# Kernel tuning notes

Hardware: AMD Instinct MI355X
Metric: run time of the kernel (lower is better)

The kernel has to match this reference:

```python
import jax, jax.numpy as jnp
import numpy as np

ITERATIONS = 10      # skil_loss default
BORDER_SIZE = 25     # skil_loss default -> 51-tap gaussian
SIGMA = 10.0         # skil_loss default
LOSS_WEIGHT = 1.0
EPS = 1e-6


def _max_pool3(x):
    # 3x3 max pool, stride 1, SAME padding over last two dims of (N, H, W)
    return jax.lax.reduce_window(x, -jnp.inf, jax.lax.max,
                                 (1, 3, 3), (1, 1, 1), 'SAME')


def _soft_erode(x):
    return -_max_pool3(-x)


def _soft_dilate(x):
    return _max_pool3(x)


def _soft_open(x):
    return _soft_dilate(_soft_erode(x))


def soft_skeletonize(img, iterations):
    # clDice-style iterative soft skeletonization
    skel = jax.nn.relu(img - _soft_open(img))

    def body(carry, _):
        img, skel = carry
        img = _soft_erode(img)
        delta = jax.nn.relu(img - _soft_open(img))
        skel = skel + jax.nn.relu(delta - skel * delta)
        return (img, skel), None

    (img, skel), _ = jax.lax.scan(body, (img, skel), None, length=iterations)
    return skel


def apply_smooth_gaussian_diffusion(x, border_size, sigma):
    # Separable gaussian conv, kernel size 2*border_size+1, peak value 1
    # (soft dilation of the skeleton into a border band), clipped to [0, 1].
    r = jnp.arange(-border_size, border_size + 1, dtype=x.dtype)
    g = jnp.exp(-(r * r) / (2.0 * sigma * sigma))  # peak = 1 at center
    x4 = x[:, None, :, :]  # (N, 1, H, W)
    kh = g.reshape(1, 1, -1, 1)
    kw = g.reshape(1, 1, 1, -1)
    dn = ('NCHW', 'OIHW', 'NCHW')
    y = jax.lax.conv_general_dilated(x4, kh, (1, 1), 'SAME', dimension_numbers=dn)
    y = jax.lax.conv_general_dilated(y, kw, (1, 1), 'SAME', dimension_numbers=dn)
    return jnp.clip(y[:, 0], 0.0, 1.0)


def soft_dice(gt, pr, epsilon=EPS):
    num = 2.0 * jnp.sum(gt * pr, axis=(-2, -1))
    den = jnp.sum(gt * gt, axis=(-2, -1)) + jnp.sum(pr * pr, axis=(-2, -1))
    return (num + epsilon) / (den + epsilon)


def skil_loss(pred_fg, target):
    gt_skel = soft_skeletonize(target, ITERATIONS)
    pr_skel = soft_skeletonize(pred_fg, ITERATIONS)
    gt_border = apply_smooth_gaussian_diffusion(gt_skel, BORDER_SIZE, SIGMA)
    pr_border = apply_smooth_gaussian_diffusion(pr_skel, BORDER_SIZE, SIGMA)
    return 1.0 - soft_dice(gt_border, pr_border)  # (N,)


def setup_inputs() -> dict:
    key = jax.random.key(0)
    k1, k2 = jax.random.split(key)
    pred = jax.random.normal(k1, (8, 2, 1024, 1024), dtype=jnp.float32)
    target = jax.random.uniform(k2, (8, 1024, 1024), dtype=jnp.float32)
    return {"pred": pred, "target": target}


def reference(pred, target):
    # SkilLoss.forward: softmax over classes, foreground channel to skil_loss,
    # weighted_loss 'mean' reduction over batch.
    probs = jax.nn.softmax(pred, axis=1)
    fg = probs[:, 1]  # (N, H, W)
    loss = skil_loss(fg, target)
    return LOSS_WEIGHT * jnp.mean(loss)
```

## Files before the change

### kernel.cpp

```cpp
#include <hip/hip_runtime.h>

#define H 1024
#define W 1024
#define HW (H*W)
#define NB 8
#define NIMG 16
#define BORDER 25
#define KLEN 51

__device__ __constant__ float GW[KLEN] = {
  0.04393693f, 0.05613476f, 0.07100535f, 0.08892162f, 0.11025053f,
  0.13533528f, 0.16447446f, 0.19789869f, 0.23574608f, 0.27803730f,
  0.32465247f, 0.37531110f, 0.42955736f, 0.48675226f, 0.54607442f,
  0.60653066f, 0.66697681f, 0.72614904f, 0.78270454f, 0.83527021f,
  0.88249690f, 0.92311635f, 0.95599748f, 0.98019867f, 0.99501248f,
  1.00000000f,
  0.99501248f, 0.98019867f, 0.95599748f, 0.92311635f, 0.88249690f,
  0.83527021f, 0.78270454f, 0.72614904f, 0.66697681f, 0.60653066f,
  0.54607442f, 0.48675226f, 0.42955736f, 0.37531110f, 0.32465247f,
  0.27803730f, 0.23574608f, 0.19789869f, 0.16447446f, 0.13533528f,
  0.11025053f, 0.08892162f, 0.07100535f, 0.05613476f, 0.04393693f
};

__device__ inline float m3n(float a,float b,float c){
  float d; asm("v_min3_f32 %0, %1, %2, %3" : "=v"(d) : "v"(a), "v"(b), "v"(c));
  return d;
}
__device__ inline float m3x(float a,float b,float c){
  float d; asm("v_max3_f32 %0, %1, %2, %3" : "=v"(d) : "v"(a), "v"(b), "v"(c));
  return d;
}

__device__ inline float dpp_shr1(float x){
  return __int_as_float(__builtin_amdgcn_mov_dpp(__float_as_int(x), 0x138, 0xf, 0xf, true));
}
__device__ inline float dpp_shl1(float x){
  return __int_as_float(__builtin_amdgcn_mov_dpp(__float_as_int(x), 0x130, 0xf, 0xf, true));
}

__device__ inline float4 hmin4(float4 C){
  float Lw = dpp_shr1(C.w);
  float Rx = dpp_shl1(C.x);
  float4 h;
  h.x=m3n(Lw ,C.x,C.y); h.y=m3n(C.x,C.y,C.z);
  h.z=m3n(C.y,C.z,C.w); h.w=m3n(C.z,C.w,Rx );
  return h;
}
__device__ inline float4 hmax4(float4 C){
  float Lw = dpp_shr1(C.w);
  float Rx = dpp_shl1(C.x);
  float4 h;
  h.x=m3x(Lw ,C.x,C.y); h.y=m3x(C.x,C.y,C.z);
  h.z=m3x(C.y,C.z,C.w); h.w=m3x(C.z,C.w,Rx );
  return h;
}
__device__ inline float4 vmin3(float4 a,float4 b,float4 c){
  float4 o; o.x=m3n(a.x,b.x,c.x); o.y=m3n(a.y,b.y,c.y);
            o.z=m3n(a.z,b.z,c.z); o.w=m3n(a.w,b.w,c.w); return o;
}
__device__ inline float4 vmax3(float4 a,float4 b,float4 c){
  float4 o; o.x=m3x(a.x,b.x,c.x); o.y=m3x(a.y,b.y,c.y);
            o.z=m3x(a.z,b.z,c.z); o.w=m3x(a.w,b.w,c.w); return o;
}
__device__ inline float4 msk4(float4 e, bool v){
  constexpr float NINF = -__builtin_huge_valf();
  float4 o; o.x=v?e.x:NINF; o.y=v?e.y:NINF; o.z=v?e.z:NINF; o.w=v?e.w:NINF;
  return o;
}

__global__ __launch_bounds__(512, 4)
void skel11_kernel(const float* __restrict__ pred, const float* __restrict__ targ,
                   float* __restrict__ S, double* __restrict__ sums)
{
  constexpr float PINF = __builtin_huge_valf();
  __shared__ float4 Xch[2][32][32];

  const int img = blockIdx.z;
  const int bx = blockIdx.x, by = blockIdx.y;

  if (bx==0 && by==0 && img==0 && threadIdx.x < 3*NB) sums[threadIdx.x] = 0.0;

  const int gx0 = bx*104 - 12, gy0 = by*72 - 12;
  const int tid = threadIdx.x;
  const int g = tid >> 5;
  const int j = tid & 31;
  const int wid = tid >> 6;
  const int R0 = 6*g;
  const int gxb = gx0 + 4*j;
  const bool xok = ((unsigned)gxb < (unsigned)W);
  const bool cenj = (j >= 3) && (j < 29);
  const bool allok = (gx0 >= 0) && (gx0 + 128 <= W) && (gy0 >= 0) && (gy0 + 96 <= H);
  const bool cwave = (wid >= 1) && (wid <= 6);

  const int ixm = (g>0)  ? 2*g-1 : 0;
  const int ixp = (g<15) ? 2*g+2 : 31;

  float4 I[6], s[6];
  bool yok[6];

  #pragma unroll
  for (int k=0;k<6;++k) {
    int gy = gy0 + R0 + k;
    yok[k] = ((unsigned)gy < (unsigned)H);
    float4 v = make_float4(PINF,PINF,PINF,PINF);
    if (yok[k] && xok) {
      size_t off = (size_t)gy*(W/4) + (gxb>>2);
      if (img < NB) {
        v = ((const float4*)targ)[(size_t)img*(HW/4)+off];
      } else {
        int b2 = img - NB;
        float4 p0 = ((const float4*)pred)[(size_t)(2*b2  )*(HW/4)+off];
        float4 p1 = ((const float4*)pred)[(size_t)(2*b2+1)*(HW/4)+off];
        v.x = 1.0f/(1.0f + expf(p0.x - p1.x));
        v.y = 1.0f/(1.0f + expf(p0.y - p1.y));
        v.z = 1.0f/(1.0f + expf(p0.z - p1.z));
        v.w = 1.0f/(1.0f + expf(p0.w - p1.w));
      }
    }
    I[k] = v;
  }

  #pragma unroll
  for (int u=0; u<11; ++u) {
    float4 h[6];
    #pragma unroll
    for (int k=0;k<6;++k) h[k] = hmin4(I[k]);
    Xch[0][2*g  ][j] = h[0];
    Xch[0][2*g+1][j] = h[5];
    __syncthreads();
    float4 hm = Xch[0][ixm][j];
    float4 hp = Xch[0][ixp][j];
    float4 e[6];
    e[0]=vmin3(hm  ,h[0],h[1]);
    e[1]=vmin3(h[0],h[1],h[2]);
    e[2]=vmin3(h[1],h[2],h[3]);
    e[3]=vmin3(h[2],h[3],h[4]);
    e[4]=vmin3(h[3],h[4],h[5]);
    e[5]=vmin3(h[4],h[5],hp  );

    float4 x[6];
    if (cwave) {
      if (allok) {
        #pragma unroll
        for (int k=0;k<6;++k) x[k] = hmax4(e[k]);
      } else {
        #pragma unroll
        for (int k=0;k<6;++k) x[k] = hmax4(msk4(e[k], xok && yok[k]));
      }
      Xch[1][2*g  ][j] = x[0];
      Xch[1][2*g+1][j] = x[5];
    } else if (wid == 0) {
      float4 x5 = allok ? hmax4(e[5]) : hmax4(msk4(e[5], xok && yok[5]));
      Xch[1][2*g+1][j] = x5;
    } else {
      float4 x0 = allok ? hmax4(e[0]) : hmax4(msk4(e[0], xok && yok[0]));
      Xch[1][2*g  ][j] = x0;
    }
    __syncthreads();

    if (cwave) {
      float4 xm = Xch[1][2*g-1][j];
      float4 xp = Xch[1][2*g+2][j];
      #pragma unroll
      for (int k=0;k<6;++k) {
        float4 dl = vmax3((k==0)?xm:x[k-1], x[k], (k==5)?xp:x[k+1]);
        float dx = fmaxf(I[k].x-dl.x,0.f), dy = fmaxf(I[k].y-dl.y,0.f);
        float dz = fmaxf(I[k].z-dl.z,0.f), dw = fmaxf(I[k].w-dl.w,0.f);
        if (u == 0) {
          s[k] = make_float4(dx,dy,dz,dw);
        } else {
          s[k].x += fmaxf(fmaf(-s[k].x, dx, dx), 0.f);
          s[k].y += fmaxf(fmaf(-s[k].y, dy, dy), 0.f);
          s[k].z += fmaxf(fmaf(-s[k].z, dz, dz), 0.f);
          s[k].w += fmaxf(fmaf(-s[k].w, dw, dw), 0.f);
        }
      }
    }
    #pragma unroll
    for (int k=0;k<6;++k) I[k] = e[k];
  }

  if (cwave && cenj && gxb < W) {
    #pragma unroll
    for (int k=0;k<6;++k) {
      int gy = gy0 + R0 + k;
      if (gy < H)
        ((float4*)S)[(size_t)img*(HW/4) + (size_t)gy*(W/4) + (gxb>>2)] = s[k];
    }
  }
}

__global__ __launch_bounds__(256)
void blur_h_kernel(const float* __restrict__ Sin, float* __restrict__ D)
{
  const int img = blockIdx.y;
  const int y = blockIdx.x;
  const int q = threadIdx.x;
  const float4* src = (const float4*)(Sin + (size_t)img*HW + (size_t)y*W);
  float a0=0.f, a1=0.f, a2=0.f, a3=0.f;
#define ACCUM(val, idx)                                                     \
  { if ((idx)   >= 0 && (idx)   <= 50) a0 += (val) * GW[(idx)];             \
    if ((idx)-1 >= 0 && (idx)-1 <= 50) a1 += (val) * GW[(idx)-1];           \
    if ((idx)-2 >= 0 && (idx)-2 <= 50) a2 += (val) * GW[(idx)-2];           \
    if ((idx)-3 >= 0 && (idx)-3 <= 50) a3 += (val) * GW[(idx)-3]; }
  #pragma unroll
  for (int c = -7; c <= 7; ++c) {
    int qq = q + c;
    float4 v = make_float4(0.f,0.f,0.f,0.f);
    if ((unsigned)qq < 256u) v = src[qq];
    const int base = 4*c + 25;
    ACCUM(v.x, base+0) ACCUM(v.y, base+1) ACCUM(v.z, base+2) ACCUM(v.w, base+3)
  }
#undef ACCUM
  float4 outv; outv.x=a0; outv.y=a1; outv.z=a2; outv.w=a3;
  ((float4*)(D + (size_t)img*HW + (size_t)y*W))[q] = outv;
}

__global__ __launch_bounds__(256)
void blur_v_dice_kernel(const float* __restrict__ D, double* __restrict__ sums)
{
  __shared__ double rbuf[12];
  const int b = blockIdx.z;
  const int gy0 = blockIdx.y * 64;
  const int gx0 = blockIdx.x * 64;
  const int tid = threadIdx.x;
  const int c  = tid & 63;
  const int r0 = gy0 + (tid >> 6) * 16;
  const int x  = gx0 + c;
  const float* gsrc = D + (size_t)b*HW + x;
  const float* psrc = D + (size_t)(b+NB)*HW + x;

  float ag[16], ap[16];
  #pragma unroll
  for (int j = 0; j < 16; ++j) { ag[j] = 0.f; ap[j] = 0.f; }
  #pragma unroll
  for (int t = 0; t < 16 + KLEN - 1; ++t) {
    int gy = r0 - BORDER + t;
    float vg = 0.f, vp = 0.f;
    if ((unsigned)gy < (unsigned)H) {
      size_t a = (size_t)gy*W;
      vg = gsrc[a]; vp = psrc[a];
    }
    #pragma unroll
    for (int j = 0; j < 16; ++j) {
      int k = t - j;
      if (k >= 0 && k < KLEN) { ag[j] += vg * GW[k]; ap[j] += vp * GW[k]; }
    }
  }
  double sgp = 0.0, sgg = 0.0, spp = 0.0;
  #pragma unroll
  for (int j = 0; j < 16; ++j) {
    float a = fminf(fmaxf(ag[j], 0.f), 1.f);
    float p = fminf(fmaxf(ap[j], 0.f), 1.f);
    sgp += (double)(a*p); sgg += (double)(a*a); spp += (double)(p*p);
  }
  #pragma unroll
  for (int off = 32; off > 0; off >>= 1) {
    sgp += __shfl_down(sgp, off);
    sgg += __shfl_down(sgg, off);
    spp += __shfl_down(spp, off);
  }
  int lane = tid & 63, wv = tid >> 6;
  if (lane == 0) { rbuf[wv] = sgp; rbuf[4+wv] = sgg; rbuf[8+wv] = spp; }
  __syncthreads();
  if (tid == 0) {
    double a  = rbuf[0]+rbuf[1]+rbuf[2]+rbuf[3];
    double g2 = rbuf[4]+rbuf[5]+rbuf[6]+rbuf[7];
    double p2 = rbuf[8]+rbuf[9]+rbuf[10]+rbuf[11];
    atomicAdd(&sums[b],        a);
    atomicAdd(&sums[NB+b],     g2);
    atomicAdd(&sums[2*NB+b],   p2);
  }
}

__global__ void final_kernel(const double* __restrict__ sums, float* __restrict__ out) {
  if (threadIdx.x == 0) {
    double acc = 0.0;
    for (int b = 0; b < NB; ++b) {
      double num = 2.0*sums[b] + 1e-6;
      double den = sums[NB+b] + sums[2*NB+b] + 1e-6;
      acc += 1.0 - num/den;
    }
    out[0] = (float)(acc / (double)NB);
  }
}

extern "C" void kernel_launch(void* const* d_in, const int* in_sizes, int n_in,
                              void* d_out, int out_size, void* d_ws, size_t ws_size,
                              hipStream_t stream)
{
  (void)in_sizes; (void)n_in; (void)out_size; (void)ws_size;
  const float* pred = (const float*)d_in[0];
  const float* targ = (const float*)d_in[1];
  float* out = (float*)d_out;

  float* Ybuf = (float*)d_ws;
  float* Sbuf = Ybuf + (size_t)NIMG*HW;
  double* sums = (double*)(Sbuf + (size_t)NIMG*HW);

  hipLaunchKernelGGL(skel11_kernel, dim3(10, 15, NIMG), dim3(512), 0, stream,
                     pred, targ, Sbuf, sums);
  hipLaunchKernelGGL(blur_h_kernel, dim3(H, NIMG), dim3(256), 0, stream, Sbuf, Ybuf);
  hipLaunchKernelGGL(blur_v_dice_kernel, dim3(W/64, H/64, NB), dim3(256), 0, stream, Ybuf, sums);
  hipLaunchKernelGGL(final_kernel, dim3(1), dim3(64), 0, stream, sums, out);
}
```

Before: 219.9 us.

## Fuse final reduction into blur_v, double rows per thread, overlap barrier work

Several changes are bundled. The final kernel launch is removed, and the last vertical-blur block, found with an atomic counter, computes the dice loss. Each blur_v thread now handles 32 rows instead of 16, which cuts the redundant halo reads of the 51-tap vertical filter but raises register pressure. The skeleton kernel moves interior-row erosion and skeleton updates before the barriers so they overlap synchronisation, and the softmax uses the fast __expf.

```diff
diff --git a/kernel.cpp b/kernel.cpp
--- a/kernel.cpp
+++ b/kernel.cpp
@@ -70,7 +70,8 @@
 
 __global__ __launch_bounds__(512, 4)
 void skel11_kernel(const float* __restrict__ pred, const float* __restrict__ targ,
-                   float* __restrict__ S, double* __restrict__ sums)
+                   float* __restrict__ S, double* __restrict__ sums,
+                   unsigned* __restrict__ cnt)
 {
   constexpr float PINF = __builtin_huge_valf();
   __shared__ float4 Xch[2][32][32];
@@ -78,7 +79,10 @@
   const int img = blockIdx.z;
   const int bx = blockIdx.x, by = blockIdx.y;
 
-  if (bx==0 && by==0 && img==0 && threadIdx.x < 3*NB) sums[threadIdx.x] = 0.0;
+  if (bx==0 && by==0 && img==0) {
+    if (threadIdx.x < 3*NB) sums[threadIdx.x] = 0.0;
+    if (threadIdx.x == 3*NB) cnt[0] = 0u;
+  }
 
   const int gx0 = bx*104 - 12, gy0 = by*72 - 12;
   const int tid = threadIdx.x;
@@ -111,10 +115,10 @@
         int b2 = img - NB;
         float4 p0 = ((const float4*)pred)[(size_t)(2*b2  )*(HW/4)+off];
         float4 p1 = ((const float4*)pred)[(size_t)(2*b2+1)*(HW/4)+off];
-        v.x = 1.0f/(1.0f + expf(p0.x - p1.x));
-        v.y = 1.0f/(1.0f + expf(p0.y - p1.y));
-        v.z = 1.0f/(1.0f + expf(p0.z - p1.z));
-        v.w = 1.0f/(1.0f + expf(p0.w - p1.w));
+        v.x = 1.0f/(1.0f + __expf(p0.x - p1.x));
+        v.y = 1.0f/(1.0f + __expf(p0.y - p1.y));
+        v.z = 1.0f/(1.0f + __expf(p0.z - p1.z));
+        v.w = 1.0f/(1.0f + __expf(p0.w - p1.w));
       }
     }
     I[k] = v;
@@ -127,15 +131,15 @@
     for (int k=0;k<6;++k) h[k] = hmin4(I[k]);
     Xch[0][2*g  ][j] = h[0];
     Xch[0][2*g+1][j] = h[5];
-    __syncthreads();
-    float4 hm = Xch[0][ixm][j];
-    float4 hp = Xch[0][ixp][j];
     float4 e[6];
-    e[0]=vmin3(hm  ,h[0],h[1]);
     e[1]=vmin3(h[0],h[1],h[2]);
     e[2]=vmin3(h[1],h[2],h[3]);
     e[3]=vmin3(h[2],h[3],h[4]);
     e[4]=vmin3(h[3],h[4],h[5]);
+    __syncthreads();
+    float4 hm = Xch[0][ixm][j];
+    float4 hp = Xch[0][ixp][j];
+    e[0]=vmin3(hm  ,h[0],h[1]);
     e[5]=vmin3(h[4],h[5],hp  );
 
     float4 x[6];
@@ -149,6 +153,20 @@
       }
       Xch[1][2*g  ][j] = x[0];
       Xch[1][2*g+1][j] = x[5];
+      #pragma unroll
+      for (int k=1;k<5;++k) {
+        float4 dl = vmax3(x[k-1], x[k], x[k+1]);
+        float dx = fmaxf(I[k].x-dl.x,0.f), dy = fmaxf(I[k].y-dl.y,0.f);
+        float dz = fmaxf(I[k].z-dl.z,0.f), dw = fmaxf(I[k].w-dl.w,0.f);
+        if (u == 0) {
+          s[k] = make_float4(dx,dy,dz,dw);
+        } else {
+          s[k].x += fmaxf(fmaf(-s[k].x, dx, dx), 0.f);
+          s[k].y += fmaxf(fmaf(-s[k].y, dy, dy), 0.f);
+          s[k].z += fmaxf(fmaf(-s[k].z, dz, dz), 0.f);
+          s[k].w += fmaxf(fmaf(-s[k].w, dw, dw), 0.f);
+        }
+      }
     } else if (wid == 0) {
       float4 x5 = allok ? hmax4(e[5]) : hmax4(msk4(e[5], xok && yok[5]));
       Xch[1][2*g+1][j] = x5;
@@ -162,8 +180,8 @@
       float4 xm = Xch[1][2*g-1][j];
       float4 xp = Xch[1][2*g+2][j];
       #pragma unroll
-      for (int k=0;k<6;++k) {
-        float4 dl = vmax3((k==0)?xm:x[k-1], x[k], (k==5)?xp:x[k+1]);
+      for (int k=0;k<6;k+=5) {
+        float4 dl = (k==0) ? vmax3(xm, x[0], x[1]) : vmax3(x[4], x[5], xp);
         float dx = fmaxf(I[k].x-dl.x,0.f), dy = fmaxf(I[k].y-dl.y,0.f);
         float dz = fmaxf(I[k].z-dl.z,0.f), dw = fmaxf(I[k].w-dl.w,0.f);
         if (u == 0) {
@@ -216,25 +234,27 @@
   ((float4*)(D + (size_t)img*HW + (size_t)y*W))[q] = outv;
 }
 
+#define NVB (16*8*NB)
 __global__ __launch_bounds__(256)
-void blur_v_dice_kernel(const float* __restrict__ D, double* __restrict__ sums)
+void blur_v_dice_kernel(const float* __restrict__ D, double* __restrict__ sums,
+                        unsigned* __restrict__ cnt, float* __restrict__ out)
 {
   __shared__ double rbuf[12];
   const int b = blockIdx.z;
-  const int gy0 = blockIdx.y * 64;
+  const int gy0 = blockIdx.y * 128;
   const int gx0 = blockIdx.x * 64;
   const int tid = threadIdx.x;
   const int c  = tid & 63;
-  const int r0 = gy0 + (tid >> 6) * 16;
+  const int r0 = gy0 + (tid >> 6) * 32;
   const int x  = gx0 + c;
   const float* gsrc = D + (size_t)b*HW + x;
   const float* psrc = D + (size_t)(b+NB)*HW + x;
 
-  float ag[16], ap[16];
-  #pragma unroll
-  for (int j = 0; j < 16; ++j) { ag[j] = 0.f; ap[j] = 0.f; }
-  #pragma unroll
-  for (int t = 0; t < 16 + KLEN - 1; ++t) {
+  float ag[32], ap[32];
+  #pragma unroll
+  for (int j = 0; j < 32; ++j) { ag[j] = 0.f; ap[j] = 0.f; }
+  #pragma unroll
+  for (int t = 0; t < 32 + KLEN - 1; ++t) {
     int gy = r0 - BORDER + t;
     float vg = 0.f, vp = 0.f;
     if ((unsigned)gy < (unsigned)H) {
@@ -242,14 +262,14 @@
       vg = gsrc[a]; vp = psrc[a];
     }
     #pragma unroll
-    for (int j = 0; j < 16; ++j) {
+    for (int j = 0; j < 32; ++j) {
       int k = t - j;
       if (k >= 0 && k < KLEN) { ag[j] += vg * GW[k]; ap[j] += vp * GW[k]; }
     }
   }
   double sgp = 0.0, sgg = 0.0, spp = 0.0;
   #pragma unroll
-  for (int j = 0; j < 16; ++j) {
+  for (int j = 0; j < 32; ++j) {
     float a = fminf(fmaxf(ag[j], 0.f), 1.f);
     float p = fminf(fmaxf(ap[j], 0.f), 1.f);
     sgp += (double)(a*p); sgg += (double)(a*a); spp += (double)(p*p);
@@ -270,18 +290,18 @@
     atomicAdd(&sums[b],        a);
     atomicAdd(&sums[NB+b],     g2);
     atomicAdd(&sums[2*NB+b],   p2);
-  }
-}
-
-__global__ void final_kernel(const double* __restrict__ sums, float* __restrict__ out) {
-  if (threadIdx.x == 0) {
-    double acc = 0.0;
-    for (int b = 0; b < NB; ++b) {
-      double num = 2.0*sums[b] + 1e-6;
-      double den = sums[NB+b] + sums[2*NB+b] + 1e-6;
-      acc += 1.0 - num/den;
-    }
-    out[0] = (float)(acc / (double)NB);
+    __threadfence();
+    unsigned done = atomicAdd(cnt, 1u);
+    if (done == NVB - 1) {
+      __threadfence();
+      double acc = 0.0;
+      for (int bb = 0; bb < NB; ++bb) {
+        double num = 2.0*sums[bb] + 1e-6;
+        double den = sums[NB+bb] + sums[2*NB+bb] + 1e-6;
+        acc += 1.0 - num/den;
+      }
+      out[0] = (float)(acc / (double)NB);
+    }
   }
 }
 
@@ -297,10 +317,11 @@
   float* Ybuf = (float*)d_ws;
   float* Sbuf = Ybuf + (size_t)NIMG*HW;
   double* sums = (double*)(Sbuf + (size_t)NIMG*HW);
+  unsigned* cnt = (unsigned*)(sums + 3*NB);
 
   hipLaunchKernelGGL(skel11_kernel, dim3(10, 15, NIMG), dim3(512), 0, stream,
-                     pred, targ, Sbuf, sums);
+                     pred, targ, Sbuf, sums, cnt);
   hipLaunchKernelGGL(blur_h_kernel, dim3(H, NIMG), dim3(256), 0, stream, Sbuf, Ybuf);
-  hipLaunchKernelGGL(blur_v_dice_kernel, dim3(W/64, H/64, NB), dim3(256), 0, stream, Ybuf, sums);
-  hipLaunchKernelGGL(final_kernel, dim3(1), dim3(64), 0, stream, sums, out);
-}
+  hipLaunchKernelGGL(blur_v_dice_kernel, dim3(W/64, H/128, NB), dim3(256), 0, stream,
+                     Ybuf, sums, cnt, out);
+}
```

Measured after the change: 640.2 us. 2.91x slower.
